# Kernel tuning notes

Measured on AMD Instinct MI355X. Metric: run time of the kernel, lower is better.

The kernel has to match this reference:

```python
import jax, jax.numpy as jnp
import numpy as np

B, S, D, C = 16, 1024, 768, 2


def setup_inputs() -> dict:
    key = jax.random.key(0)
    ks = jax.random.split(key, 6)
    sc = 1.0 / np.sqrt(D)
    return {
        "tokens": jax.random.normal(ks[0], (B, S, D), jnp.float32),
        "Wk": jax.random.normal(ks[1], (D, D), jnp.float32) * sc,
        "bk": jnp.zeros((D,), jnp.float32),
        "Wq": jax.random.normal(ks[2], (D, D), jnp.float32) * sc,
        "bq": jnp.zeros((D,), jnp.float32),
        "Wv": jax.random.normal(ks[3], (D, D), jnp.float32) * sc,
        "bv": jnp.zeros((D,), jnp.float32),
        "ln_g": jnp.ones((S, D), jnp.float32),
        "ln_b": jnp.zeros((S, D), jnp.float32),
        "W_sgsa": jax.random.normal(ks[4], (D, 1), jnp.float32) * sc,
        "b_sgsa": jnp.zeros((1,), jnp.float32),
        "W_fnn": jax.random.normal(ks[5], (4 * D, C), jnp.float32) * (1.0 / np.sqrt(4 * D)),
        "b_fnn": jnp.zeros((C,), jnp.float32),
    }


def reference(tokens, Wk, bk, Wq, bq, Wv, bv, ln_g, ln_b, W_sgsa, b_sgsa, W_fnn, b_fnn):
    fact = 1.0 / jnp.sqrt(jnp.asarray(D, tokens.dtype))
    # --- token-wise single-head attention ---
    K = tokens @ Wk + bk                                  # [B,S,D]
    Q = tokens @ Wq + bq
    V = tokens @ Wv + bv
    att = jax.nn.softmax(jnp.einsum('bsd,btd->bst', Q, K) * fact, axis=-1)  # [B,S,S]
    out = jnp.einsum('bst,btd->bsd', att, V)              # [B,S,D]
    # --- LayerNorm over last two dims (S,D) jointly, eps=1e-8 ---
    mu = jnp.mean(out, axis=(1, 2), keepdims=True)
    var = jnp.var(out, axis=(1, 2), keepdims=True)
    out_ln = (out - mu) / jnp.sqrt(var + 1e-8) * ln_g + ln_b
    # --- feature-wise attention (same K/Q/V weights, transposed bmm) ---
    K_N = out_ln @ Wk + bk
    Q_N = out_ln @ Wq + bq
    V_N = out_ln @ Wv + bv
    att_N = jax.nn.softmax(jnp.einsum('bsd,bse->bde', Q_N, K_N) * fact, axis=-1)  # [B,D,D]
    out_N = jnp.einsum('bsd,bde->bse', V_N, att_N)        # [B,S,D]
    # --- SGSA gating ---
    gate = out_N @ W_sgsa + b_sgsa                        # [B,S,1]
    out_sgsa = gate * out_N                               # [B,S,D]
    # --- concat, dual pooling, FC ---
    cat = jnp.concatenate([tokens, out_sgsa], axis=2)     # [B,S,2D]
    pooled = jnp.concatenate([jnp.mean(cat, axis=1), jnp.max(cat, axis=1)], axis=1)  # [B,4D]
    return pooled @ W_fnn + b_fnn                         # [B,C]
```

## Files before the change

kernel.cpp:

```cpp
#include <hip/hip_runtime.h>

#define BB 16
#define SS 1024
#define DD 768

typedef _Float16 f16x4 __attribute__((ext_vector_type(4)));
typedef _Float16 f16x8 __attribute__((ext_vector_type(8)));
typedef float f32x4 __attribute__((ext_vector_type(4)));

__device__ __forceinline__ void gload_lds16(const void* g, void* l) {
  __builtin_amdgcn_global_load_lds(
      (const __attribute__((address_space(1))) unsigned int*)g,
      (__attribute__((address_space(3))) unsigned int*)l, 16, 0, 0);
}

template<int OUTM, int BIAS>
__global__ __launch_bounds__(256) void gemm_f16(
    const _Float16* __restrict__ A, long long aB,
    const _Float16* __restrict__ Bt, long long bB,
    const float* __restrict__ bias, int biasB,
    void* __restrict__ Cv, long long cB,
    int M, int N, int K)
{
  __shared__ __attribute__((aligned(16))) _Float16 lA[128 * 32];
  __shared__ __attribute__((aligned(16))) _Float16 lB[128 * 32];

  const int t = threadIdx.x;
  const int z = blockIdx.z;
  const _Float16* Ab = A + (size_t)z * aB;
  const _Float16* Bb = Bt + (size_t)z * bB;
  const int m0 = blockIdx.x * 128, n0 = blockIdx.y * 128;
  const int l = t & 63, w = t >> 6;
  const int wr = (w >> 1) * 64, wc = (w & 1) * 64;
  const int lrow = l & 15, lkb = (l >> 4) * 8;

  f32x4 acc[4][4] = {};

  const size_t ldaB = (size_t)K * 2;
  const int o0 = t * 16;
  const int o1 = o0 + 4096;
  const int rA0 = o0 >> 6, cb0 = o0 & 63;
  const int rA1 = o1 >> 6, cb1 = o1 & 63;

  for (int k0 = 0; k0 < K; k0 += 32) {
    const char* ga = (const char*)Ab + (size_t)k0 * 2;
    const char* gb = (const char*)Bb + (size_t)k0 * 2;
    gload_lds16(ga + (size_t)(m0 + rA0) * ldaB + cb0, (char*)lA + o0);
    gload_lds16(ga + (size_t)(m0 + rA1) * ldaB + cb1, (char*)lA + o1);
    gload_lds16(gb + (size_t)(n0 + rA0) * ldaB + cb0, (char*)lB + o0);
    gload_lds16(gb + (size_t)(n0 + rA1) * ldaB + cb1, (char*)lB + o1);
    __syncthreads();

    f16x8 af[4], bfr[4];
    #pragma unroll
    for (int m = 0; m < 4; m++) af[m]  = *(const f16x8*)&lA[(wr + m * 16 + lrow) * 32 + lkb];
    #pragma unroll
    for (int n = 0; n < 4; n++) bfr[n] = *(const f16x8*)&lB[(wc + n * 16 + lrow) * 32 + lkb];
    #pragma unroll
    for (int m = 0; m < 4; m++)
      #pragma unroll
      for (int n = 0; n < 4; n++)
        acc[m][n] = __builtin_amdgcn_mfma_f32_16x16x32_f16(af[m], bfr[n], acc[m][n], 0, 0, 0);
    __syncthreads();
  }

  const int crow = (l >> 4) * 4, ccol = l & 15;
  #pragma unroll
  for (int m = 0; m < 4; m++) {
    const int rq = m0 + wr + m * 16 + crow;
    #pragma unroll
    for (int n = 0; n < 4; n++) {
      const int c = n0 + wc + n * 16 + ccol;
      const float bv = BIAS ? bias[(size_t)z * biasB + c] : 0.0f;
      if (OUTM == 0) {
        float* C = (float*)Cv + (size_t)z * cB;
        #pragma unroll
        for (int j = 0; j < 4; j++)
          C[(size_t)(rq + j) * N + c] = acc[m][n][j] + bv;
      } else if (OUTM == 1) {
        _Float16* C = (_Float16*)Cv + (size_t)z * cB;
        #pragma unroll
        for (int j = 0; j < 4; j++)
          C[(size_t)(rq + j) * N + c] = (_Float16)(acc[m][n][j] + bv);
      } else {
        _Float16* C = (_Float16*)Cv + (size_t)z * cB;
        const int bq = rq >> 10, s = rq & 1023;
        f16x4 o;
        #pragma unroll
        for (int j = 0; j < 4; j++) o[j] = (_Float16)(acc[m][n][j] + bv);
        *(f16x4*)&C[((size_t)(bq * N + c) << 10) + s] = o;
      }
    }
  }
}

__global__ __launch_bounds__(256) void cast_f2h(const float* __restrict__ in,
                                                _Float16* __restrict__ outp, long long n4)
{
  for (long long i = (long long)blockIdx.x * 256 + threadIdx.x; i < n4;
       i += (long long)gridDim.x * 256) {
    float4 v = ((const float4*)in)[i];
    f16x4 r;
    r[0] = (_Float16)v.x; r[1] = (_Float16)v.y; r[2] = (_Float16)v.z; r[3] = (_Float16)v.w;
    ((f16x4*)outp)[i] = r;
  }
}

__global__ __launch_bounds__(256) void transpose_f2h(const float* __restrict__ in,
                                                     _Float16* __restrict__ outp, int R, int C)
{
  __shared__ float tile[32][33];
  const int r0 = blockIdx.y * 32, c0 = blockIdx.x * 32;
  const int tx = threadIdx.x & 31, ty = threadIdx.x >> 5;
  #pragma unroll
  for (int i = 0; i < 4; i++)
    tile[ty + i * 8][tx] = in[(size_t)(r0 + ty + i * 8) * C + c0 + tx];
  __syncthreads();
  #pragma unroll
  for (int i = 0; i < 4; i++)
    outp[(size_t)(c0 + ty + i * 8) * R + r0 + tx] = (_Float16)tile[tx][ty + i * 8];
}

__global__ __launch_bounds__(256) void transpose_b2h(const _Float16* __restrict__ in, long long inB,
                                                     _Float16* __restrict__ outp, long long outB,
                                                     int R, int C)
{
  __shared__ _Float16 tile[32][33];
  const _Float16* ib = in + (size_t)blockIdx.z * inB;
  _Float16* ob = outp + (size_t)blockIdx.z * outB;
  const int r0 = blockIdx.y * 32, c0 = blockIdx.x * 32;
  const int tx = threadIdx.x & 31, ty = threadIdx.x >> 5;
  #pragma unroll
  for (int i = 0; i < 4; i++)
    tile[ty + i * 8][tx] = ib[(size_t)(r0 + ty + i * 8) * C + c0 + tx];
  __syncthreads();
  #pragma unroll
  for (int i = 0; i < 4; i++)
    ob[(size_t)(c0 + ty + i * 8) * R + r0 + tx] = tile[tx][ty + i * 8];
}

__global__ void pack2_k(const float* __restrict__ a, const float* __restrict__ b,
                        float* __restrict__ o)
{
  int t = blockIdx.x * 256 + threadIdx.x;
  if (t < 768) o[t] = a[t];
  else if (t < 1536) o[t] = b[t - 768];
}

template<int VPT>
__global__ __launch_bounds__(256) void softmax_f2h(const float* __restrict__ X,
                                                   _Float16* __restrict__ Y,
                                                   int L, float scale)
{
  const size_t base = (size_t)blockIdx.x * L;
  const int t = threadIdx.x;
  float v[VPT];
  float m = -3.4e38f;
  #pragma unroll
  for (int j = 0; j < VPT; j++) { v[j] = X[base + t + j * 256]; m = fmaxf(m, v[j]); }
  __shared__ float red[256];
  red[t] = m; __syncthreads();
  #pragma unroll
  for (int off = 128; off > 0; off >>= 1) {
    if (t < off) red[t] = fmaxf(red[t], red[t + off]);
    __syncthreads();
  }
  m = red[0]; __syncthreads();
  float s = 0.0f;
  #pragma unroll
  for (int j = 0; j < VPT; j++) { v[j] = __expf((v[j] - m) * scale); s += v[j]; }
  red[t] = s; __syncthreads();
  #pragma unroll
  for (int off = 128; off > 0; off >>= 1) {
    if (t < off) red[t] += red[t + off];
    __syncthreads();
  }
  const float inv = 1.0f / red[0];
  #pragma unroll
  for (int j = 0; j < VPT; j++) Y[base + t + j * 256] = (_Float16)(v[j] * inv);
}

__global__ __launch_bounds__(256) void ln_partial(const float* __restrict__ src,
                                                  float* __restrict__ part)
{
  const int b = blockIdx.y, ch = blockIdx.x;
  const float4* p = (const float4*)(src + (size_t)b * SS * DD) + (size_t)ch * 3072;
  const int t = threadIdx.x;
  float s = 0.0f, q = 0.0f;
  #pragma unroll
  for (int i = 0; i < 12; i++) {
    float4 v = p[t + i * 256];
    s += v.x + v.y + v.z + v.w;
    q += v.x * v.x + v.y * v.y + v.z * v.z + v.w * v.w;
  }
  __shared__ float rs[256], rq[256];
  rs[t] = s; rq[t] = q; __syncthreads();
  #pragma unroll
  for (int off = 128; off > 0; off >>= 1) {
    if (t < off) { rs[t] += rs[t + off]; rq[t] += rq[t + off]; }
    __syncthreads();
  }
  if (t == 0) { part[(b * 64 + ch) * 2] = rs[0]; part[(b * 64 + ch) * 2 + 1] = rq[0]; }
}

__global__ void ln_final(const float* __restrict__ part, float* __restrict__ stats)
{
  const int b = blockIdx.x, t = threadIdx.x;
  float s = part[(b * 64 + t) * 2];
  float q = part[(b * 64 + t) * 2 + 1];
  #pragma unroll
  for (int off = 32; off > 0; off >>= 1) { s += __shfl_down(s, off); q += __shfl_down(q, off); }
  if (t == 0) {
    const float invN = 1.0f / (float)(SS * DD);
    float mu = s * invN;
    float var = q * invN - mu * mu;
    stats[b * 2] = mu;
    stats[b * 2 + 1] = rsqrtf(var + 1e-8f);
  }
}

__global__ __launch_bounds__(256) void ln_apply_h(const float* __restrict__ src,
                                                  const float* __restrict__ g,
                                                  const float* __restrict__ bta,
                                                  const float* __restrict__ stats,
                                                  _Float16* __restrict__ dst)
{
  const long long n4 = (long long)BB * SS * DD / 4;
  const int SD4 = SS * DD / 4;
  for (long long i = (long long)blockIdx.x * 256 + threadIdx.x; i < n4;
       i += (long long)gridDim.x * 256) {
    const int b = (int)(i / SD4);
    const int sd4 = (int)(i - (long long)b * SD4);
    const float mu = stats[b * 2], rs = stats[b * 2 + 1];
    float4 v = ((const float4*)src)[i];
    float4 gg = ((const float4*)g)[sd4];
    float4 bb = ((const float4*)bta)[sd4];
    f16x4 r;
    r[0] = (_Float16)((v.x - mu) * rs * gg.x + bb.x);
    r[1] = (_Float16)((v.y - mu) * rs * gg.y + bb.y);
    r[2] = (_Float16)((v.z - mu) * rs * gg.z + bb.z);
    r[3] = (_Float16)((v.w - mu) * rs * gg.w + bb.w);
    ((f16x4*)dst)[i] = r;
  }
}

__global__ __launch_bounds__(256) void gate_k(const float* __restrict__ outN,
                                              const float* __restrict__ wsg,
                                              const float* __restrict__ bsg,
                                              float* __restrict__ gate)
{
  const int row = blockIdx.x * 4 + (threadIdx.x >> 6);
  const int l = threadIdx.x & 63;
  const float* src = outN + (size_t)row * DD;
  float s = 0.0f;
  #pragma unroll
  for (int i = 0; i < 12; i++) s += src[l + i * 64] * wsg[l + i * 64];
  #pragma unroll
  for (int off = 32; off > 0; off >>= 1) s += __shfl_down(s, off);
  if (l == 0) gate[row] = s + bsg[0];
}

__global__ __launch_bounds__(256) void pool_partial(const float* __restrict__ tokens,
                                                    const float* __restrict__ outN,
                                                    const float* __restrict__ gate,
                                                    float* __restrict__ part)
{
  const int b = blockIdx.y, ch = blockIdx.x, t = threadIdx.x;
  float st0 = 0, st1 = 0, st2 = 0, so0 = 0, so1 = 0, so2 = 0;
  float xt0 = -3.4e38f, xt1 = -3.4e38f, xt2 = -3.4e38f;
  float xo0 = -3.4e38f, xo1 = -3.4e38f, xo2 = -3.4e38f;
  const size_t rowbase = ((size_t)b * SS + ch * 64) * DD;
  for (int i = 0; i < 64; i++) {
    const float* tr = tokens + rowbase + (size_t)i * DD;
    const float* orw = outN + rowbase + (size_t)i * DD;
    const float g = gate[b * SS + ch * 64 + i];
    float t0 = tr[t], t1 = tr[t + 256], t2 = tr[t + 512];
    float o0 = orw[t] * g, o1 = orw[t + 256] * g, o2 = orw[t + 512] * g;
    st0 += t0; st1 += t1; st2 += t2;
    so0 += o0; so1 += o1; so2 += o2;
    xt0 = fmaxf(xt0, t0); xt1 = fmaxf(xt1, t1); xt2 = fmaxf(xt2, t2);
    xo0 = fmaxf(xo0, o0); xo1 = fmaxf(xo1, o1); xo2 = fmaxf(xo2, o2);
  }
  float* pb = part + (size_t)(b * 16 + ch) * 3072;
  pb[t] = st0;          pb[t + 256] = st1;          pb[t + 512] = st2;
  pb[768 + t] = so0;    pb[768 + t + 256] = so1;    pb[768 + t + 512] = so2;
  pb[1536 + t] = xt0;   pb[1536 + t + 256] = xt1;   pb[1536 + t + 512] = xt2;
  pb[2304 + t] = xo0;   pb[2304 + t + 256] = xo1;   pb[2304 + t + 512] = xo2;
}

__global__ __launch_bounds__(256) void pool_final(const float* __restrict__ part,
                                                  float* __restrict__ pooled)
{
  const int idx = blockIdx.x * 256 + threadIdx.x;
  const int b = idx / DD, d = idx - b * DD;
  float st = 0, so = 0, xt = -3.4e38f, xo = -3.4e38f;
  for (int ch = 0; ch < 16; ch++) {
    const float* pb = part + (size_t)(b * 16 + ch) * 3072;
    st += pb[d]; so += pb[768 + d];
    xt = fmaxf(xt, pb[1536 + d]); xo = fmaxf(xo, pb[2304 + d]);
  }
  const float inv = 1.0f / (float)SS;
  pooled[(size_t)b * 3072 + d]        = st * inv;
  pooled[(size_t)b * 3072 + 768 + d]  = so * inv;
  pooled[(size_t)b * 3072 + 1536 + d] = xt;
  pooled[(size_t)b * 3072 + 2304 + d] = xo;
}

__global__ __launch_bounds__(256) void fc_k(const float* __restrict__ pooled,
                                            const float* __restrict__ Wf,
                                            const float* __restrict__ bf,
                                            float* __restrict__ outp)
{
  const int b = blockIdx.x, t = threadIdx.x;
  float p0 = 0.0f, p1 = 0.0f;
  #pragma unroll
  for (int i = 0; i < 12; i++) {
    const int j = t + i * 256;
    const float pv = pooled[(size_t)b * 3072 + j];
    p0 += pv * Wf[j * 2];
    p1 += pv * Wf[j * 2 + 1];
  }
  __shared__ float r0[256], r1[256];
  r0[t] = p0; r1[t] = p1; __syncthreads();
  #pragma unroll
  for (int off = 128; off > 0; off >>= 1) {
    if (t < off) { r0[t] += r0[t + off]; r1[t] += r1[t + off]; }
    __syncthreads();
  }
  if (t == 0) {
    outp[b * 2 + 0] = r0[0] + bf[0];
    outp[b * 2 + 1] = r1[0] + bf[1];
  }
}

extern "C" void kernel_launch(void* const* d_in, const int* in_sizes, int n_in,
                              void* d_out, int out_size, void* d_ws, size_t ws_size,
                              hipStream_t stream)
{
  const float* tokens = (const float*)d_in[0];
  const float* Wk  = (const float*)d_in[1];
  const float* bk  = (const float*)d_in[2];
  const float* Wq  = (const float*)d_in[3];
  const float* bq  = (const float*)d_in[4];
  const float* Wv  = (const float*)d_in[5];
  const float* bv  = (const float*)d_in[6];
  const float* lng = (const float*)d_in[7];
  const float* lnb = (const float*)d_in[8];
  const float* Wsg = (const float*)d_in[9];
  const float* bsg = (const float*)d_in[10];
  const float* Wf  = (const float*)d_in[11];
  const float* bfn = (const float*)d_in[12];
  float* outp = (float*)d_out;
  (void)in_sizes; (void)n_in; (void)out_size; (void)ws_size;

  char* ws = (char*)d_ws;
  float*    R0   = (float*)(ws + 0);
  _Float16* R1   = (_Float16*)(ws + 67108864);
  _Float16* R2   = (_Float16*)(ws + 92274688);
  _Float16* R3   = (_Float16*)(ws + 117440512);
  _Float16* R4   = (_Float16*)(ws + 142606336);
  _Float16* R5   = (_Float16*)(ws + 167772160);
  _Float16* Wt   = (_Float16*)(ws + 201326592);
  float* pack2   = (float*)(ws + 204865536);
  float* part    = (float*)(ws + 204871680);
  float* stats   = (float*)(ws + 204879872);
  float* gate    = (float*)(ws + 204880000);
  float* ppart   = (float*)(ws + 204945536);
  float* pooled  = (float*)(ws + 208091264);

  const float fact = 0.036084391824351615f;
  const long long SD = (long long)SS * DD;
  const long long S2 = (long long)SS * SS;
  const long long D2 = (long long)DD * DD;
  const long long PL = (long long)BB * SD;

  cast_f2h<<<2048, 256, 0, stream>>>(tokens, R1, PL / 4);
  transpose_f2h<<<dim3(24, 24), 256, 0, stream>>>(Wk, Wt,               768, 768);
  transpose_f2h<<<dim3(24, 24), 256, 0, stream>>>(Wq, Wt + 589824,      768, 768);
  transpose_f2h<<<dim3(24, 24), 256, 0, stream>>>(Wv, Wt + 2 * 589824,  768, 768);
  pack2_k<<<6, 256, 0, stream>>>(bk, bq, pack2);

  gemm_f16<1, 1><<<dim3(128, 6, 2), 256, 0, stream>>>(R1, 0, Wt, 589824, pack2, 768,
                                                      (void*)R2, PL, BB * SS, DD, DD);
  gemm_f16<2, 1><<<dim3(128, 6, 1), 256, 0, stream>>>(R1, 0, Wt + 2 * 589824, 0, bv, 0,
                                                      (void*)R4, 0, BB * SS, DD, DD);

  gemm_f16<0, 0><<<dim3(8, 8, 16), 256, 0, stream>>>(R3, SD, R2, SD, nullptr, 0,
                                                     (void*)R0, S2, SS, SS, DD);
  softmax_f2h<4><<<BB * SS, 256, 0, stream>>>(R0, R5, SS, fact);
  gemm_f16<0, 0><<<dim3(8, 6, 16), 256, 0, stream>>>(R5, S2, R4, SD, nullptr, 0,
                                                     (void*)R0, SD, SS, DD, SS);
  ln_partial<<<dim3(64, 16), 256, 0, stream>>>(R0, part);
  ln_final<<<16, 64, 0, stream>>>(part, stats);
  ln_apply_h<<<2048, 256, 0, stream>>>(R0, lng, lnb, stats, R1);

  gemm_f16<2, 1><<<dim3(128, 6, 2), 256, 0, stream>>>(R1, 0, Wt, 589824, pack2, 768,
                                                      (void*)R2, PL, BB * SS, DD, DD);
  gemm_f16<1, 1><<<dim3(128, 6, 1), 256, 0, stream>>>(R1, 0, Wt + 2 * 589824, 0, bv, 0,
                                                      (void*)R4, 0, BB * SS, DD, DD);

  gemm_f16<0, 0><<<dim3(6, 6, 16), 256, 0, stream>>>(R3, SD, R2, SD, nullptr, 0,
                                                     (void*)R0, D2, DD, DD, SS);
  softmax_f2h<3><<<BB * DD, 256, 0, stream>>>(R0, R5, DD, fact);
  transpose_b2h<<<dim3(24, 24, 16), 256, 0, stream>>>(R5, D2, R1, D2, DD, DD);
  gemm_f16<0, 0><<<dim3(8, 6, 16), 256, 0, stream>>>(R4, SD, R1, D2, nullptr, 0,
                                                     (void*)R0, SD, SS, DD, DD);

  gate_k<<<4096, 256, 0, stream>>>(R0, Wsg, bsg, gate);
  pool_partial<<<dim3(16, BB), 256, 0, stream>>>(tokens, R0, gate, ppart);
  pool_final<<<48, 256, 0, stream>>>(ppart, pooled);
  fc_k<<<16, 256, 0, stream>>>(pooled, Wf, bfn, outp);
}
```

Measured before the change: 500.1 us.

## Replace GEMM with 256x256-tile, 4-stage async-LDS pipelined kernel and fuse QKV projections

Replaces the 128x128 single-buffered GEMM with a 512-thread 256x256-tile kernel. It prefetches three K-slices ahead into a 4-deep LDS ring using global_load_lds, syncs with explicit vmcnt waits and a barrier, and raises wave priority around the MFMA block. The three Q/K/V projections become one launch with a packed bias, and each output's layout (row-major or transposed) is chosen per z. Pooling partials are also split into twice as many chunks for more parallelism. The goal is to hide global memory latency and raise reuse per loaded byte. In exchange, far fewer blocks are launched (for example 144 for the feature-wise score GEMM), which risks underfilling the CUs, and the 128KB of LDS allows only one block per CU.

After: 601.7 us. 1.2x slower.

```diff
diff --git a/kernel.cpp b/kernel.cpp
--- a/kernel.cpp
+++ b/kernel.cpp
@@ -15,61 +15,88 @@
 }
 
 template<int OUTM, int BIAS>
-__global__ __launch_bounds__(256) void gemm_f16(
+__global__ __launch_bounds__(512) void gemm256(
     const _Float16* __restrict__ A, long long aB,
     const _Float16* __restrict__ Bt, long long bB,
     const float* __restrict__ bias, int biasB,
     void* __restrict__ Cv, long long cB,
     int M, int N, int K)
 {
-  __shared__ __attribute__((aligned(16))) _Float16 lA[128 * 32];
-  __shared__ __attribute__((aligned(16))) _Float16 lB[128 * 32];
-
+  __shared__ __attribute__((aligned(16))) _Float16 lds[65536];
   const int t = threadIdx.x;
   const int z = blockIdx.z;
+  const int m0 = blockIdx.x * 256, n0 = blockIdx.y * 256;
   const _Float16* Ab = A + (size_t)z * aB;
   const _Float16* Bb = Bt + (size_t)z * bB;
-  const int m0 = blockIdx.x * 128, n0 = blockIdx.y * 128;
+
+  const int rr = t & 255, kb0 = t >> 8;
+  const char* gA = (const char*)(Ab + (size_t)(m0 + rr) * K) + kb0 * 16;
+  const char* gB = (const char*)(Bb + (size_t)(n0 + rr) * K) + kb0 * 16;
+  char* const ldsb = (char*)lds;
+  const int d0 = t * 16;
+
+  const int NTk = K >> 5;
+
+  #pragma unroll
+  for (int p = 0; p < 3; ++p) {
+    char* la = ldsb + p * 32768;
+    const char* ga = gA + p * 64;
+    const char* gb = gB + p * 64;
+    gload_lds16(ga,      la + d0);
+    gload_lds16(ga + 32, la + 8192 + d0);
+    gload_lds16(gb,      la + 16384 + d0);
+    gload_lds16(gb + 32, la + 24576 + d0);
+  }
+
   const int l = t & 63, w = t >> 6;
-  const int wr = (w >> 1) * 64, wc = (w & 1) * 64;
-  const int lrow = l & 15, lkb = (l >> 4) * 8;
-
-  f32x4 acc[4][4] = {};
-
-  const size_t ldaB = (size_t)K * 2;
-  const int o0 = t * 16;
-  const int o1 = o0 + 4096;
-  const int rA0 = o0 >> 6, cb0 = o0 & 63;
-  const int rA1 = o1 >> 6, cb1 = o1 & 63;
-
-  for (int k0 = 0; k0 < K; k0 += 32) {
-    const char* ga = (const char*)Ab + (size_t)k0 * 2;
-    const char* gb = (const char*)Bb + (size_t)k0 * 2;
-    gload_lds16(ga + (size_t)(m0 + rA0) * ldaB + cb0, (char*)lA + o0);
-    gload_lds16(ga + (size_t)(m0 + rA1) * ldaB + cb1, (char*)lA + o1);
-    gload_lds16(gb + (size_t)(n0 + rA0) * ldaB + cb0, (char*)lB + o0);
-    gload_lds16(gb + (size_t)(n0 + rA1) * ldaB + cb1, (char*)lB + o1);
-    __syncthreads();
-
-    f16x8 af[4], bfr[4];
+  const int wr = (w >> 2) * 128, wc = (w & 3) * 64;
+  const int lrow = l & 15, kq = l >> 4;
+
+  f32x4 acc[8][4] = {};
+
+  for (int tt = 0; tt < NTk; ++tt) {
+    const int rem = NTk - 1 - tt;
+    if (rem >= 2)      asm volatile("s_waitcnt vmcnt(8)" ::: "memory");
+    else if (rem == 1) asm volatile("s_waitcnt vmcnt(4)" ::: "memory");
+    else               asm volatile("s_waitcnt vmcnt(0)" ::: "memory");
+    __builtin_amdgcn_s_barrier();
+    asm volatile("" ::: "memory");
+
+    if (tt + 3 < NTk) {
+      char* la = ldsb + ((tt + 3) & 3) * 32768;
+      const char* ga = gA + (size_t)(tt + 3) * 64;
+      const char* gb = gB + (size_t)(tt + 3) * 64;
+      gload_lds16(ga,      la + d0);
+      gload_lds16(ga + 32, la + 8192 + d0);
+      gload_lds16(gb,      la + 16384 + d0);
+      gload_lds16(gb + 32, la + 24576 + d0);
+    }
+
+    const _Float16* la = (const _Float16*)(ldsb + (tt & 3) * 32768);
+    const _Float16* lb = la + 8192;
+    f16x8 bfr[4], af[8];
     #pragma unroll
-    for (int m = 0; m < 4; m++) af[m]  = *(const f16x8*)&lA[(wr + m * 16 + lrow) * 32 + lkb];
+    for (int n = 0; n < 4; ++n)
+      bfr[n] = *(const f16x8*)&lb[kq * 2048 + (wc + n * 16 + lrow) * 8];
     #pragma unroll
-    for (int n = 0; n < 4; n++) bfr[n] = *(const f16x8*)&lB[(wc + n * 16 + lrow) * 32 + lkb];
+    for (int m = 0; m < 8; ++m)
+      af[m] = *(const f16x8*)&la[kq * 2048 + (wr + m * 16 + lrow) * 8];
+
+    __builtin_amdgcn_s_setprio(1);
     #pragma unroll
-    for (int m = 0; m < 4; m++)
+    for (int m = 0; m < 8; ++m)
       #pragma unroll
-      for (int n = 0; n < 4; n++)
+      for (int n = 0; n < 4; ++n)
         acc[m][n] = __builtin_amdgcn_mfma_f32_16x16x32_f16(af[m], bfr[n], acc[m][n], 0, 0, 0);
-    __syncthreads();
+    __builtin_amdgcn_s_setprio(0);
   }
 
   const int crow = (l >> 4) * 4, ccol = l & 15;
   #pragma unroll
-  for (int m = 0; m < 4; m++) {
+  for (int m = 0; m < 8; ++m) {
     const int rq = m0 + wr + m * 16 + crow;
     #pragma unroll
-    for (int n = 0; n < 4; n++) {
+    for (int n = 0; n < 4; ++n) {
       const int c = n0 + wc + n * 16 + ccol;
       const float bv = BIAS ? bias[(size_t)z * biasB + c] : 0.0f;
       if (OUTM == 0) {
@@ -77,18 +104,20 @@
         #pragma unroll
         for (int j = 0; j < 4; j++)
           C[(size_t)(rq + j) * N + c] = acc[m][n][j] + bv;
-      } else if (OUTM == 1) {
-        _Float16* C = (_Float16*)Cv + (size_t)z * cB;
-        #pragma unroll
-        for (int j = 0; j < 4; j++)
-          C[(size_t)(rq + j) * N + c] = (_Float16)(acc[m][n][j] + bv);
       } else {
         _Float16* C = (_Float16*)Cv + (size_t)z * cB;
-        const int bq = rq >> 10, s = rq & 1023;
-        f16x4 o;
-        #pragma unroll
-        for (int j = 0; j < 4; j++) o[j] = (_Float16)(acc[m][n][j] + bv);
-        *(f16x4*)&C[((size_t)(bq * N + c) << 10) + s] = o;
+        const bool tr = (OUTM == 3) ? (z == 2) : (z < 2);
+        if (tr) {
+          const int bq = rq >> 10, s = rq & 1023;
+          f16x4 o;
+          #pragma unroll
+          for (int j = 0; j < 4; j++) o[j] = (_Float16)(acc[m][n][j] + bv);
+          *(f16x4*)&C[((size_t)(bq * N + c) << 10) + s] = o;
+        } else {
+          #pragma unroll
+          for (int j = 0; j < 4; j++)
+            C[(size_t)(rq + j) * N + c] = (_Float16)(acc[m][n][j] + bv);
+        }
       }
     }
   }
@@ -139,12 +168,13 @@
     ob[(size_t)(c0 + ty + i * 8) * R + r0 + tx] = tile[tx][ty + i * 8];
 }
 
-__global__ void pack2_k(const float* __restrict__ a, const float* __restrict__ b,
-                        float* __restrict__ o)
+__global__ void pack_bias(const float* __restrict__ a, const float* __restrict__ b,
+                          const float* __restrict__ c, float* __restrict__ o)
 {
   int t = blockIdx.x * 256 + threadIdx.x;
   if (t < 768) o[t] = a[t];
   else if (t < 1536) o[t] = b[t - 768];
+  else if (t < 2304) o[t] = c[t - 1536];
 }
 
 template<int VPT>
@@ -269,11 +299,11 @@
   float st0 = 0, st1 = 0, st2 = 0, so0 = 0, so1 = 0, so2 = 0;
   float xt0 = -3.4e38f, xt1 = -3.4e38f, xt2 = -3.4e38f;
   float xo0 = -3.4e38f, xo1 = -3.4e38f, xo2 = -3.4e38f;
-  const size_t rowbase = ((size_t)b * SS + ch * 64) * DD;
-  for (int i = 0; i < 64; i++) {
+  const size_t rowbase = ((size_t)b * SS + ch * 32) * DD;
+  for (int i = 0; i < 32; i++) {
     const float* tr = tokens + rowbase + (size_t)i * DD;
     const float* orw = outN + rowbase + (size_t)i * DD;
-    const float g = gate[b * SS + ch * 64 + i];
+    const float g = gate[b * SS + ch * 32 + i];
     float t0 = tr[t], t1 = tr[t + 256], t2 = tr[t + 512];
     float o0 = orw[t] * g, o1 = orw[t + 256] * g, o2 = orw[t + 512] * g;
     st0 += t0; st1 += t1; st2 += t2;
@@ -281,7 +311,7 @@
     xt0 = fmaxf(xt0, t0); xt1 = fmaxf(xt1, t1); xt2 = fmaxf(xt2, t2);
     xo0 = fmaxf(xo0, o0); xo1 = fmaxf(xo1, o1); xo2 = fmaxf(xo2, o2);
   }
-  float* pb = part + (size_t)(b * 16 + ch) * 3072;
+  float* pb = part + (size_t)(b * 32 + ch) * 3072;
   pb[t] = st0;          pb[t + 256] = st1;          pb[t + 512] = st2;
   pb[768 + t] = so0;    pb[768 + t + 256] = so1;    pb[768 + t + 512] = so2;
   pb[1536 + t] = xt0;   pb[1536 + t + 256] = xt1;   pb[1536 + t + 512] = xt2;
@@ -294,8 +324,8 @@
   const int idx = blockIdx.x * 256 + threadIdx.x;
   const int b = idx / DD, d = idx - b * DD;
   float st = 0, so = 0, xt = -3.4e38f, xo = -3.4e38f;
-  for (int ch = 0; ch < 16; ch++) {
-    const float* pb = part + (size_t)(b * 16 + ch) * 3072;
+  for (int ch = 0; ch < 32; ch++) {
+    const float* pb = part + (size_t)(b * 32 + ch) * 3072;
     st += pb[d]; so += pb[768 + d];
     xt = fmaxf(xt, pb[1536 + d]); xo = fmaxf(xo, pb[2304 + d]);
   }
@@ -361,12 +391,12 @@
   _Float16* R4   = (_Float16*)(ws + 142606336);
   _Float16* R5   = (_Float16*)(ws + 167772160);
   _Float16* Wt   = (_Float16*)(ws + 201326592);
-  float* pack2   = (float*)(ws + 204865536);
-  float* part    = (float*)(ws + 204871680);
-  float* stats   = (float*)(ws + 204879872);
-  float* gate    = (float*)(ws + 204880000);
-  float* ppart   = (float*)(ws + 204945536);
-  float* pooled  = (float*)(ws + 208091264);
+  float* bias3   = (float*)(ws + 204865536);
+  float* part    = (float*)(ws + 204874752);
+  float* stats   = (float*)(ws + 204882944);
+  float* gate    = (float*)(ws + 204883072);
+  float* ppart   = (float*)(ws + 204948608);
+  float* pooled  = (float*)(ws + 211240064);
 
   const float fact = 0.036084391824351615f;
   const long long SD = (long long)SS * DD;
@@ -378,36 +408,30 @@
   transpose_f2h<<<dim3(24, 24), 256, 0, stream>>>(Wk, Wt,               768, 768);
   transpose_f2h<<<dim3(24, 24), 256, 0, stream>>>(Wq, Wt + 589824,      768, 768);
   transpose_f2h<<<dim3(24, 24), 256, 0, stream>>>(Wv, Wt + 2 * 589824,  768, 768);
-  pack2_k<<<6, 256, 0, stream>>>(bk, bq, pack2);
-
-  gemm_f16<1, 1><<<dim3(128, 6, 2), 256, 0, stream>>>(R1, 0, Wt, 589824, pack2, 768,
-                                                      (void*)R2, PL, BB * SS, DD, DD);
-  gemm_f16<2, 1><<<dim3(128, 6, 1), 256, 0, stream>>>(R1, 0, Wt + 2 * 589824, 0, bv, 0,
-                                                      (void*)R4, 0, BB * SS, DD, DD);
-
-  gemm_f16<0, 0><<<dim3(8, 8, 16), 256, 0, stream>>>(R3, SD, R2, SD, nullptr, 0,
-                                                     (void*)R0, S2, SS, SS, DD);
+  pack_bias<<<9, 256, 0, stream>>>(bk, bq, bv, bias3);
+
+  gemm256<3, 1><<<dim3(64, 3, 3), 512, 0, stream>>>(R1, 0, Wt, 589824, bias3, 768,
+                                                    (void*)R2, PL, BB * SS, DD, DD);
+  gemm256<0, 0><<<dim3(4, 4, 16), 512, 0, stream>>>(R3, SD, R2, SD, nullptr, 0,
+                                                    (void*)R0, S2, SS, SS, DD);
   softmax_f2h<4><<<BB * SS, 256, 0, stream>>>(R0, R5, SS, fact);
-  gemm_f16<0, 0><<<dim3(8, 6, 16), 256, 0, stream>>>(R5, S2, R4, SD, nullptr, 0,
-                                                     (void*)R0, SD, SS, DD, SS);
+  gemm256<0, 0><<<dim3(4, 3, 16), 512, 0, stream>>>(R5, S2, R4, SD, nullptr, 0,
+                                                    (void*)R0, SD, SS, DD, SS);
   ln_partial<<<dim3(64, 16), 256, 0, stream>>>(R0, part);
   ln_final<<<16, 64, 0, stream>>>(part, stats);
   ln_apply_h<<<2048, 256, 0, stream>>>(R0, lng, lnb, stats, R1);
 
-  gemm_f16<2, 1><<<dim3(128, 6, 2), 256, 0, stream>>>(R1, 0, Wt, 589824, pack2, 768,
-                                                      (void*)R2, PL, BB * SS, DD, DD);
-  gemm_f16<1, 1><<<dim3(128, 6, 1), 256, 0, stream>>>(R1, 0, Wt + 2 * 589824, 0, bv, 0,
-                                                      (void*)R4, 0, BB * SS, DD, DD);
-
-  gemm_f16<0, 0><<<dim3(6, 6, 16), 256, 0, stream>>>(R3, SD, R2, SD, nullptr, 0,
-                                                     (void*)R0, D2, DD, DD, SS);
+  gemm256<4, 1><<<dim3(64, 3, 3), 512, 0, stream>>>(R1, 0, Wt, 589824, bias3, 768,
+                                                    (void*)R2, PL, BB * SS, DD, DD);
+  gemm256<0, 0><<<dim3(3, 3, 16), 512, 0, stream>>>(R3, SD, R2, SD, nullptr, 0,
+                                                    (void*)R0, D2, DD, DD, SS);
   softmax_f2h<3><<<BB * DD, 256, 0, stream>>>(R0, R5, DD, fact);
   transpose_b2h<<<dim3(24, 24, 16), 256, 0, stream>>>(R5, D2, R1, D2, DD, DD);
-  gemm_f16<0, 0><<<dim3(8, 6, 16), 256, 0, stream>>>(R4, SD, R1, D2, nullptr, 0,
-                                                     (void*)R0, SD, SS, DD, DD);
+  gemm256<0, 0><<<dim3(4, 3, 16), 512, 0, stream>>>(R4, SD, R1, D2, nullptr, 0,
+                                                    (void*)R0, SD, SS, DD, DD);
 
   gate_k<<<4096, 256, 0, stream>>>(R0, Wsg, bsg, gate);
-  pool_partial<<<dim3(16, BB), 256, 0, stream>>>(tokens, R0, gate, ppart);
+  pool_partial<<<dim3(32, BB), 256, 0, stream>>>(tokens, R0, gate, ppart);
   pool_final<<<48, 256, 0, stream>>>(ppart, pooled);
   fc_k<<<16, 256, 0, stream>>>(pooled, Wf, bfn, outp);
 }
```
